# Performance work log

Hardware: AMD Instinct MI355X
Metric: run time of the kernel (lower is better)

Reference implementation:

```python
import jax, jax.numpy as jnp
import numpy as np

N = 50000
E = 800000
D = 128
NCLASS = 10


def setup_inputs() -> dict:
    key = jax.random.key(0)
    ks = jax.random.split(key, 12)
    stdv = 1.0 / np.sqrt(D)
    inp = {
        "x": jax.random.normal(ks[0], (N, D), dtype=jnp.float32),
        "edge_src": jax.random.randint(ks[1], (E,), 0, N, dtype=jnp.int32),
        "edge_dst": jax.random.randint(ks[2], (E,), 0, N, dtype=jnp.int32),
        "edge_weight": jax.random.uniform(ks[3], (E,), dtype=jnp.float32),
        "W1": jax.random.uniform(ks[4], (D, D), jnp.float32, -stdv, stdv),
        "b1": jax.random.uniform(ks[5], (D,), jnp.float32, -stdv, stdv),
        "W2": jax.random.uniform(ks[6], (D, D), jnp.float32, -stdv, stdv),
        "b2": jax.random.uniform(ks[7], (D,), jnp.float32, -stdv, stdv),
        "W3": jax.random.uniform(ks[8], (D, D), jnp.float32, -stdv, stdv),
        "b3": jax.random.uniform(ks[9], (D,), jnp.float32, -stdv, stdv),
        "lin_W": jax.random.normal(ks[10], (NCLASS, 3 * D), dtype=jnp.float32) * 0.05,
        "lin_b": jax.random.normal(ks[11], (NCLASS,), dtype=jnp.float32) * 0.05,
    }
    return inp


def _gcn_layer(h, W, b, edge_src, edge_dst, edge_weight):
    # support = h @ W  (dense GEMM), then spmm(adj, support) as gather-scale-scatter
    support = h @ W                                   # [N, out]
    msgs = support[edge_src] * edge_weight[:, None]   # [E, out]
    agg = jax.ops.segment_sum(msgs, edge_dst, num_segments=h.shape[0])
    return agg + b


def reference(x, edge_src, edge_dst, edge_weight, W1, b1, W2, b2, W3, b3, lin_W, lin_b):
    x1 = jax.nn.relu(_gcn_layer(x, W1, b1, edge_src, edge_dst, edge_weight))
    o1 = jnp.max(x1, axis=0)
    x2 = jax.nn.relu(_gcn_layer(x1, W2, b2, edge_src, edge_dst, edge_weight))
    o2 = jnp.max(x2, axis=0)
    x3 = _gcn_layer(x2, W3, b3, edge_src, edge_dst, edge_weight)
    o3 = jnp.max(x3, axis=0)
    lin_in = jnp.concatenate([o1, o2, o3], axis=0)    # [3*D]
    logits = lin_W @ lin_in + lin_b                   # [nclass]
    return jax.nn.log_softmax(logits, axis=0)
```

## Files before the change

### kernel.cpp

```cpp
#include <hip/hip_runtime.h>
#include <hip/hip_bf16.h>
#include <math.h>

#define NN 50000
#define NPAD 50048
#define NE 800000
#define DD 128
#define NCLS 10
#define SCAN_BLOCK 1024
#define NTILES ((NN + 1 + SCAN_BLOCK - 1) / SCAN_BLOCK)

typedef short s16x8 __attribute__((ext_vector_type(8)));
typedef float f32x4 __attribute__((ext_vector_type(4)));

__device__ __forceinline__ unsigned short f2bf(float x) {
  __hip_bfloat16 h = __float2bfloat16(x);
  return __builtin_bit_cast(unsigned short, h);
}

__device__ __forceinline__ unsigned int fkey(float f) {
  unsigned int u = __float_as_uint(f);
  return u ^ ((u & 0x80000000u) ? 0xFFFFFFFFu : 0x80000000u);
}
__device__ __forceinline__ float funkey(unsigned int k) {
  unsigned int u = (k & 0x80000000u) ? (k ^ 0x80000000u) : ~k;
  return __uint_as_float(u);
}

__global__ void k_init(int* __restrict__ offs, unsigned int* __restrict__ omax) {
  int i = blockIdx.x * blockDim.x + threadIdx.x;
  if (i < NN + 1) offs[i] = 0;
  if (i < 3 * DD) omax[i] = 0u;
}

__global__ void k_count(const int* __restrict__ edst, int* __restrict__ offs) {
  int e = blockIdx.x * blockDim.x + threadIdx.x;
  if (e < NE) atomicAdd(&offs[edst[e] + 1], 1);
}

__global__ void k_scan_partial(const int* __restrict__ offs, int* __restrict__ bsum) {
  __shared__ int red[SCAN_BLOCK];
  int i = blockIdx.x * SCAN_BLOCK + threadIdx.x;
  red[threadIdx.x] = (i < NN + 1) ? offs[i] : 0;
  __syncthreads();
  for (int off = SCAN_BLOCK / 2; off > 0; off >>= 1) {
    if ((int)threadIdx.x < off) red[threadIdx.x] += red[threadIdx.x + off];
    __syncthreads();
  }
  if (threadIdx.x == 0) bsum[blockIdx.x] = red[0];
}

__global__ void k_scan_bsum(int* __restrict__ bsum) {
  if (threadIdx.x == 0) {
    int run = 0;
    for (int i = 0; i < NTILES; ++i) { int v = bsum[i]; bsum[i] = run; run += v; }
  }
}

__global__ void k_scan_final(int* __restrict__ offs, const int* __restrict__ bsum,
                             int* __restrict__ cursor) {
  __shared__ int tmp[SCAN_BLOCK];
  int i = blockIdx.x * SCAN_BLOCK + threadIdx.x;
  int v = (i < NN + 1) ? offs[i] : 0;
  tmp[threadIdx.x] = v;
  __syncthreads();
  for (int off = 1; off < SCAN_BLOCK; off <<= 1) {
    int t = ((int)threadIdx.x >= off) ? tmp[threadIdx.x - off] : 0;
    __syncthreads();
    tmp[threadIdx.x] += t;
    __syncthreads();
  }
  int incl = tmp[threadIdx.x] + bsum[blockIdx.x];
  if (i < NN + 1) {
    offs[i] = incl;
    if (i < NN) cursor[i] = incl;
  }
}

__global__ void k_fill(const int* __restrict__ esrc, const int* __restrict__ edst,
                       const float* __restrict__ ew, int* __restrict__ cursor,
                       int2* __restrict__ csr) {
  int e = blockIdx.x * blockDim.x + threadIdx.x;
  if (e < NE) {
    int d = edst[e];
    int p = atomicAdd(&cursor[d], 1);
    csr[p] = make_int2(esrc[e], __float_as_int(ew[e]));
  }
}

__global__ __launch_bounds__(256) void k_cvt(const float* __restrict__ x,
                     const float* __restrict__ W1, const float* __restrict__ W2,
                     const float* __restrict__ W3,
                     unsigned short* __restrict__ HB,
                     unsigned short* __restrict__ WT1, unsigned short* __restrict__ WT2,
                     unsigned short* __restrict__ WT3) {
  const int stride = gridDim.x * 256;
  int i = blockIdx.x * 256 + threadIdx.x;
  const int n4 = NPAD * DD / 4;
  const int nx4 = NN * DD / 4;
  for (int idx = i; idx < n4; idx += stride) {
    float4 v = make_float4(0.f, 0.f, 0.f, 0.f);
    if (idx < nx4) v = ((const float4*)x)[idx];
    ushort2 lo = make_ushort2(f2bf(v.x), f2bf(v.y));
    ushort2 hi = make_ushort2(f2bf(v.z), f2bf(v.w));
    uint2 pv = make_uint2((uint)lo.x | ((uint)lo.y << 16), (uint)hi.x | ((uint)hi.y << 16));
    *(uint2*)&HB[idx * 4] = pv;
  }
  if (i < DD * DD) {
    int k = i >> 7, c = i & 127;
    WT1[c * DD + k] = f2bf(W1[i]);
    WT2[c * DD + k] = f2bf(W2[i]);
    WT3[c * DD + k] = f2bf(W3[i]);
  }
}

__global__ __launch_bounds__(256) void k_mm(const unsigned short* __restrict__ H,
                                            const unsigned short* __restrict__ Wt,
                                            unsigned short* __restrict__ S) {
  const int wave = threadIdx.x >> 6, lane = threadIdx.x & 63;
  const int gw = blockIdx.x * 4 + wave;
  const int r0 = (gw >> 1) * 64;
  const int cbase = (gw & 1) * 64;
  const int l15 = lane & 15, lk = (lane >> 4) * 8;

  s16x8 Af[4][4];
  s16x8 Bf[4][4];
#pragma unroll
  for (int m = 0; m < 4; ++m)
#pragma unroll
    for (int ks = 0; ks < 4; ++ks)
      Af[m][ks] = *(const s16x8*)&Wt[(cbase + m * 16 + l15) * DD + ks * 32 + lk];
#pragma unroll
  for (int n = 0; n < 4; ++n)
#pragma unroll
    for (int ks = 0; ks < 4; ++ks)
      Bf[n][ks] = *(const s16x8*)&H[(size_t)(r0 + n * 16 + l15) * DD + ks * 32 + lk];

  f32x4 acc[4][4];
#pragma unroll
  for (int m = 0; m < 4; ++m)
#pragma unroll
    for (int n = 0; n < 4; ++n) acc[m][n] = (f32x4){0.f, 0.f, 0.f, 0.f};

#pragma unroll
  for (int ks = 0; ks < 4; ++ks)
#pragma unroll
    for (int m = 0; m < 4; ++m)
#pragma unroll
      for (int n = 0; n < 4; ++n)
        acc[m][n] = __builtin_amdgcn_mfma_f32_16x16x32_bf16(Af[m][ks], Bf[n][ks],
                                                            acc[m][n], 0, 0, 0);

  const int csub = 4 * (lane >> 4);
#pragma unroll
  for (int m = 0; m < 4; ++m)
#pragma unroll
    for (int n = 0; n < 4; ++n) {
      uint2 pv;
      pv.x = (uint)f2bf(acc[m][n][0]) | ((uint)f2bf(acc[m][n][1]) << 16);
      pv.y = (uint)f2bf(acc[m][n][2]) | ((uint)f2bf(acc[m][n][3]) << 16);
      *(uint2*)&S[(size_t)(r0 + n * 16 + l15) * DD + cbase + m * 16 + csub] = pv;
    }
}

__global__ __launch_bounds__(256) void k_agg(const unsigned short* __restrict__ S,
                                             const int2* __restrict__ csr,
                                             const int* __restrict__ offs,
                                             const float* __restrict__ bias,
                                             unsigned short* __restrict__ Xout,
                                             unsigned int* __restrict__ omax,
                                             int do_relu) {
  __shared__ unsigned int cmax[DD];
  for (int i = threadIdx.x; i < DD; i += 256) cmax[i] = 0u;
  __syncthreads();
  const int lane = threadIdx.x & 63;
  const int wave = threadIdx.x >> 6;
  const int gwave = blockIdx.x * 4 + wave;
  const int nwaves = gridDim.x * 4;
  const int c0 = lane * 2;
  const float2 b2 = *(const float2*)&bias[c0];
  float2 mx = make_float2(-INFINITY, -INFINITY);
  for (int d = gwave; d < NN; d += nwaves) {
    const int e1 = offs[d + 1];
    int e = offs[d];
    float2 acc = b2;
    for (; e + 4 <= e1; e += 4) {
      int2 sw0 = csr[e + 0];
      int2 sw1 = csr[e + 1];
      int2 sw2 = csr[e + 2];
      int2 sw3 = csr[e + 3];
      unsigned int u0 = *(const unsigned int*)&S[(size_t)sw0.x * DD + c0];
      unsigned int u1 = *(const unsigned int*)&S[(size_t)sw1.x * DD + c0];
      unsigned int u2 = *(const unsigned int*)&S[(size_t)sw2.x * DD + c0];
      unsigned int u3 = *(const unsigned int*)&S[(size_t)sw3.x * DD + c0];
      float w0 = __int_as_float(sw0.y), w1 = __int_as_float(sw1.y);
      float w2 = __int_as_float(sw2.y), w3 = __int_as_float(sw3.y);
      acc.x = fmaf(w0, __uint_as_float(u0 << 16), acc.x);
      acc.y = fmaf(w0, __uint_as_float(u0 & 0xFFFF0000u), acc.y);
      acc.x = fmaf(w1, __uint_as_float(u1 << 16), acc.x);
      acc.y = fmaf(w1, __uint_as_float(u1 & 0xFFFF0000u), acc.y);
      acc.x = fmaf(w2, __uint_as_float(u2 << 16), acc.x);
      acc.y = fmaf(w2, __uint_as_float(u2 & 0xFFFF0000u), acc.y);
      acc.x = fmaf(w3, __uint_as_float(u3 << 16), acc.x);
      acc.y = fmaf(w3, __uint_as_float(u3 & 0xFFFF0000u), acc.y);
    }
    for (; e < e1; ++e) {
      int2 sw = csr[e];
      float w = __int_as_float(sw.y);
      unsigned int u = *(const unsigned int*)&S[(size_t)sw.x * DD + c0];
      acc.x = fmaf(w, __uint_as_float(u << 16), acc.x);
      acc.y = fmaf(w, __uint_as_float(u & 0xFFFF0000u), acc.y);
    }
    if (do_relu) { acc.x = fmaxf(acc.x, 0.f); acc.y = fmaxf(acc.y, 0.f); }
    if (Xout) {
      unsigned int xu = (unsigned int)f2bf(acc.x) | ((unsigned int)f2bf(acc.y) << 16);
      *(unsigned int*)&Xout[(size_t)d * DD + c0] = xu;
    }
    mx.x = fmaxf(mx.x, acc.x);
    mx.y = fmaxf(mx.y, acc.y);
  }
  atomicMax(&cmax[c0], fkey(mx.x));
  atomicMax(&cmax[c0 + 1], fkey(mx.y));
  __syncthreads();
  for (int i = threadIdx.x; i < DD; i += 256) atomicMax(&omax[i], cmax[i]);
}

__global__ void k_head(const unsigned int* __restrict__ omax,
                       const float* __restrict__ linW,
                       const float* __restrict__ linb,
                       float* __restrict__ out) {
  __shared__ float o[3 * DD];
  __shared__ float logits[NCLS];
  int t = threadIdx.x;
  if (t < 3 * DD) o[t] = funkey(omax[t]);
  __syncthreads();
  if (t < NCLS) {
    float acc = linb[t];
    for (int j = 0; j < 3 * DD; ++j) acc = fmaf(linW[t * 3 * DD + j], o[j], acc);
    logits[t] = acc;
  }
  __syncthreads();
  if (t == 0) {
    float m = -INFINITY;
    for (int c = 0; c < NCLS; ++c) m = fmaxf(m, logits[c]);
    float s = 0.f;
    for (int c = 0; c < NCLS; ++c) s += expf(logits[c] - m);
    float ls = logf(s);
    for (int c = 0; c < NCLS; ++c) out[c] = logits[c] - m - ls;
  }
}

extern "C" void kernel_launch(void* const* d_in, const int* in_sizes, int n_in,
                              void* d_out, int out_size, void* d_ws, size_t ws_size,
                              hipStream_t stream) {
  const float* x    = (const float*)d_in[0];
  const int*   esrc = (const int*)d_in[1];
  const int*   edst = (const int*)d_in[2];
  const float* ew   = (const float*)d_in[3];
  const float* W1   = (const float*)d_in[4];
  const float* b1   = (const float*)d_in[5];
  const float* W2   = (const float*)d_in[6];
  const float* b2   = (const float*)d_in[7];
  const float* W3   = (const float*)d_in[8];
  const float* b3   = (const float*)d_in[9];
  const float* linW = (const float*)d_in[10];
  const float* linb = (const float*)d_in[11];
  float* out = (float*)d_out;

  size_t off = 0;
  auto alloc = [&](size_t bytes) {
    void* p = (char*)d_ws + off;
    off += (bytes + 255) & ~(size_t)255;
    return p;
  };
  unsigned short* HB   = (unsigned short*)alloc((size_t)NPAD * DD * 2);
  unsigned short* XB   = (unsigned short*)alloc((size_t)NPAD * DD * 2);
  unsigned short* S    = (unsigned short*)alloc((size_t)NPAD * DD * 2);
  unsigned short* WT1  = (unsigned short*)alloc((size_t)DD * DD * 2);
  unsigned short* WT2  = (unsigned short*)alloc((size_t)DD * DD * 2);
  unsigned short* WT3  = (unsigned short*)alloc((size_t)DD * DD * 2);
  int*          offs   = (int*)alloc((NN + 1) * 4);
  int*          cursor = (int*)alloc(NN * 4);
  int2*         csr    = (int2*)alloc((size_t)NE * 8);
  unsigned int* omax   = (unsigned int*)alloc(3 * DD * 4);
  int*          bsum   = (int*)alloc(NTILES * 4);
  (void)ws_size; (void)n_in; (void)in_sizes; (void)out_size;

  k_init<<<(NN + 256) / 256, 256, 0, stream>>>(offs, omax);
  k_count<<<(NE + 255) / 256, 256, 0, stream>>>(edst, offs);
  k_scan_partial<<<NTILES, SCAN_BLOCK, 0, stream>>>(offs, bsum);
  k_scan_bsum<<<1, 64, 0, stream>>>(bsum);
  k_scan_final<<<NTILES, SCAN_BLOCK, 0, stream>>>(offs, bsum, cursor);
  k_fill<<<(NE + 255) / 256, 256, 0, stream>>>(esrc, edst, ew, cursor, csr);

  k_cvt<<<2048, 256, 0, stream>>>(x, W1, W2, W3, HB, WT1, WT2, WT3);

  const int mm_grid = (NPAD / 64) * 2 / 4;
  k_mm<<<mm_grid, 256, 0, stream>>>(HB, WT1, S);
  k_agg<<<2048, 256, 0, stream>>>(S, csr, offs, b1, XB, omax, 1);
  k_mm<<<mm_grid, 256, 0, stream>>>(XB, WT2, S);
  k_agg<<<2048, 256, 0, stream>>>(S, csr, offs, b2, HB, omax + DD, 1);
  k_mm<<<mm_grid, 256, 0, stream>>>(HB, WT3, S);
  k_agg<<<2048, 256, 0, stream>>>(S, csr, offs, b3, nullptr, omax + 2 * DD, 0);

  k_head<<<1, 384, 0, stream>>>(omax, linW, linb, out);
}
```

Baseline: 440.5 us.

## Fuse x bf16 conversion into GEMM, halve GEMM tile, widen aggregation gathers

Removes the separate pass that converts x to bf16 and folds that conversion into the first GEMM's operand load, which saves one full read and write of the node features. The GEMM tile per wave shrinks from 64 to 32 rows, doubling the grid and lowering register use. The aggregation kernel now gives each quarter-wave a different edge and has each lane gather 16 bytes, then combines the quarters with cross-lane shuffles. This trades a few shuffles per node and a ragged tail loop for fewer, wider gather transactions.

```diff
diff --git a/kernel.cpp b/kernel.cpp
--- a/kernel.cpp
+++ b/kernel.cpp
@@ -17,6 +17,8 @@
   __hip_bfloat16 h = __float2bfloat16(x);
   return __builtin_bit_cast(unsigned short, h);
 }
+__device__ __forceinline__ float bflo(unsigned int u) { return __uint_as_float(u << 16); }
+__device__ __forceinline__ float bfhi(unsigned int u) { return __uint_as_float(u & 0xFFFF0000u); }
 
 __device__ __forceinline__ unsigned int fkey(float f) {
   unsigned int u = __float_as_uint(f);
@@ -88,24 +90,11 @@
   }
 }
 
-__global__ __launch_bounds__(256) void k_cvt(const float* __restrict__ x,
-                     const float* __restrict__ W1, const float* __restrict__ W2,
-                     const float* __restrict__ W3,
-                     unsigned short* __restrict__ HB,
-                     unsigned short* __restrict__ WT1, unsigned short* __restrict__ WT2,
-                     unsigned short* __restrict__ WT3) {
-  const int stride = gridDim.x * 256;
+__global__ __launch_bounds__(256) void k_cvtW(const float* __restrict__ W1,
+    const float* __restrict__ W2, const float* __restrict__ W3,
+    unsigned short* __restrict__ WT1, unsigned short* __restrict__ WT2,
+    unsigned short* __restrict__ WT3) {
   int i = blockIdx.x * 256 + threadIdx.x;
-  const int n4 = NPAD * DD / 4;
-  const int nx4 = NN * DD / 4;
-  for (int idx = i; idx < n4; idx += stride) {
-    float4 v = make_float4(0.f, 0.f, 0.f, 0.f);
-    if (idx < nx4) v = ((const float4*)x)[idx];
-    ushort2 lo = make_ushort2(f2bf(v.x), f2bf(v.y));
-    ushort2 hi = make_ushort2(f2bf(v.z), f2bf(v.w));
-    uint2 pv = make_uint2((uint)lo.x | ((uint)lo.y << 16), (uint)hi.x | ((uint)hi.y << 16));
-    *(uint2*)&HB[idx * 4] = pv;
-  }
   if (i < DD * DD) {
     int k = i >> 7, c = i & 127;
     WT1[c * DD + k] = f2bf(W1[i]);
@@ -114,40 +103,63 @@
   }
 }
 
-__global__ __launch_bounds__(256) void k_mm(const unsigned short* __restrict__ H,
+template <int F32IN>
+__global__ __launch_bounds__(256) void k_mm(const void* __restrict__ Hv,
                                             const unsigned short* __restrict__ Wt,
                                             unsigned short* __restrict__ S) {
   const int wave = threadIdx.x >> 6, lane = threadIdx.x & 63;
   const int gw = blockIdx.x * 4 + wave;
-  const int r0 = (gw >> 1) * 64;
+  const int r0 = (gw >> 1) * 32;
   const int cbase = (gw & 1) * 64;
   const int l15 = lane & 15, lk = (lane >> 4) * 8;
 
   s16x8 Af[4][4];
-  s16x8 Bf[4][4];
 #pragma unroll
   for (int m = 0; m < 4; ++m)
 #pragma unroll
     for (int ks = 0; ks < 4; ++ks)
       Af[m][ks] = *(const s16x8*)&Wt[(cbase + m * 16 + l15) * DD + ks * 32 + lk];
-#pragma unroll
-  for (int n = 0; n < 4; ++n)
-#pragma unroll
-    for (int ks = 0; ks < 4; ++ks)
-      Bf[n][ks] = *(const s16x8*)&H[(size_t)(r0 + n * 16 + l15) * DD + ks * 32 + lk];
-
-  f32x4 acc[4][4];
+
+  s16x8 Bf[2][4];
+#pragma unroll
+  for (int n = 0; n < 2; ++n) {
+    const int r = r0 + n * 16 + l15;
+    if (F32IN) {
+      const float* H = (const float*)Hv;
+#pragma unroll
+      for (int ks = 0; ks < 4; ++ks) {
+        float4 a = make_float4(0.f, 0.f, 0.f, 0.f), b = a;
+        if (r < NN) {
+          a = *(const float4*)&H[(size_t)r * DD + ks * 32 + lk];
+          b = *(const float4*)&H[(size_t)r * DD + ks * 32 + lk + 4];
+        }
+        s16x8 f;
+        f[0] = (short)f2bf(a.x); f[1] = (short)f2bf(a.y);
+        f[2] = (short)f2bf(a.z); f[3] = (short)f2bf(a.w);
+        f[4] = (short)f2bf(b.x); f[5] = (short)f2bf(b.y);
+        f[6] = (short)f2bf(b.z); f[7] = (short)f2bf(b.w);
+        Bf[n][ks] = f;
+      }
+    } else {
+      const unsigned short* H = (const unsigned short*)Hv;
+#pragma unroll
+      for (int ks = 0; ks < 4; ++ks)
+        Bf[n][ks] = *(const s16x8*)&H[(size_t)r * DD + ks * 32 + lk];
+    }
+  }
+
+  f32x4 acc[4][2];
 #pragma unroll
   for (int m = 0; m < 4; ++m)
 #pragma unroll
-    for (int n = 0; n < 4; ++n) acc[m][n] = (f32x4){0.f, 0.f, 0.f, 0.f};
+    for (int n = 0; n < 2; ++n) acc[m][n] = (f32x4){0.f, 0.f, 0.f, 0.f};
 
 #pragma unroll
   for (int ks = 0; ks < 4; ++ks)
 #pragma unroll
     for (int m = 0; m < 4; ++m)
 #pragma unroll
-      for (int n = 0; n < 4; ++n)
+      for (int n = 0; n < 2; ++n)
         acc[m][n] = __builtin_amdgcn_mfma_f32_16x16x32_bf16(Af[m][ks], Bf[n][ks],
                                                             acc[m][n], 0, 0, 0);
 
@@ -155,12 +167,23 @@
 #pragma unroll
   for (int m = 0; m < 4; ++m)
 #pragma unroll
-    for (int n = 0; n < 4; ++n) {
+    for (int n = 0; n < 2; ++n) {
       uint2 pv;
       pv.x = (uint)f2bf(acc[m][n][0]) | ((uint)f2bf(acc[m][n][1]) << 16);
       pv.y = (uint)f2bf(acc[m][n][2]) | ((uint)f2bf(acc[m][n][3]) << 16);
       *(uint2*)&S[(size_t)(r0 + n * 16 + l15) * DD + cbase + m * 16 + csub] = pv;
     }
+}
+
+__device__ __forceinline__ void fma8(float* acc, float w, uint4 u) {
+  acc[0] = fmaf(w, bflo(u.x), acc[0]);
+  acc[1] = fmaf(w, bfhi(u.x), acc[1]);
+  acc[2] = fmaf(w, bflo(u.y), acc[2]);
+  acc[3] = fmaf(w, bfhi(u.y), acc[3]);
+  acc[4] = fmaf(w, bflo(u.z), acc[4]);
+  acc[5] = fmaf(w, bfhi(u.z), acc[5]);
+  acc[6] = fmaf(w, bflo(u.w), acc[6]);
+  acc[7] = fmaf(w, bfhi(u.w), acc[7]);
 }
 
 __global__ __launch_bounds__(256) void k_agg(const unsigned short* __restrict__ S,
@@ -175,52 +198,70 @@
   __syncthreads();
   const int lane = threadIdx.x & 63;
   const int wave = threadIdx.x >> 6;
+  const int q = lane >> 4;
+  const int t = lane & 15;
   const int gwave = blockIdx.x * 4 + wave;
   const int nwaves = gridDim.x * 4;
-  const int c0 = lane * 2;
-  const float2 b2 = *(const float2*)&bias[c0];
-  float2 mx = make_float2(-INFINITY, -INFINITY);
+
+  float bcol[8];
+  {
+    float4 b0 = *(const float4*)&bias[t * 8];
+    float4 b1 = *(const float4*)&bias[t * 8 + 4];
+    bcol[0] = b0.x; bcol[1] = b0.y; bcol[2] = b0.z; bcol[3] = b0.w;
+    bcol[4] = b1.x; bcol[5] = b1.y; bcol[6] = b1.z; bcol[7] = b1.w;
+  }
+  float mx[8];
+#pragma unroll
+  for (int j = 0; j < 8; ++j) mx[j] = -INFINITY;
+
   for (int d = gwave; d < NN; d += nwaves) {
-    const int e1 = offs[d + 1];
-    int e = offs[d];
-    float2 acc = b2;
-    for (; e + 4 <= e1; e += 4) {
-      int2 sw0 = csr[e + 0];
-      int2 sw1 = csr[e + 1];
-      int2 sw2 = csr[e + 2];
-      int2 sw3 = csr[e + 3];
-      unsigned int u0 = *(const unsigned int*)&S[(size_t)sw0.x * DD + c0];
-      unsigned int u1 = *(const unsigned int*)&S[(size_t)sw1.x * DD + c0];
-      unsigned int u2 = *(const unsigned int*)&S[(size_t)sw2.x * DD + c0];
-      unsigned int u3 = *(const unsigned int*)&S[(size_t)sw3.x * DD + c0];
-      float w0 = __int_as_float(sw0.y), w1 = __int_as_float(sw1.y);
-      float w2 = __int_as_float(sw2.y), w3 = __int_as_float(sw3.y);
-      acc.x = fmaf(w0, __uint_as_float(u0 << 16), acc.x);
-      acc.y = fmaf(w0, __uint_as_float(u0 & 0xFFFF0000u), acc.y);
-      acc.x = fmaf(w1, __uint_as_float(u1 << 16), acc.x);
-      acc.y = fmaf(w1, __uint_as_float(u1 & 0xFFFF0000u), acc.y);
-      acc.x = fmaf(w2, __uint_as_float(u2 << 16), acc.x);
-      acc.y = fmaf(w2, __uint_as_float(u2 & 0xFFFF0000u), acc.y);
-      acc.x = fmaf(w3, __uint_as_float(u3 << 16), acc.x);
-      acc.y = fmaf(w3, __uint_as_float(u3 & 0xFFFF0000u), acc.y);
-    }
-    for (; e < e1; ++e) {
-      int2 sw = csr[e];
-      float w = __int_as_float(sw.y);
-      unsigned int u = *(const unsigned int*)&S[(size_t)sw.x * DD + c0];
-      acc.x = fmaf(w, __uint_as_float(u << 16), acc.x);
-      acc.y = fmaf(w, __uint_as_float(u & 0xFFFF0000u), acc.y);
-    }
-    if (do_relu) { acc.x = fmaxf(acc.x, 0.f); acc.y = fmaxf(acc.y, 0.f); }
-    if (Xout) {
-      unsigned int xu = (unsigned int)f2bf(acc.x) | ((unsigned int)f2bf(acc.y) << 16);
-      *(unsigned int*)&Xout[(size_t)d * DD + c0] = xu;
-    }
-    mx.x = fmaxf(mx.x, acc.x);
-    mx.y = fmaxf(mx.y, acc.y);
-  }
-  atomicMax(&cmax[c0], fkey(mx.x));
-  atomicMax(&cmax[c0 + 1], fkey(mx.y));
+    const int e0 = offs[d], e1 = offs[d + 1];
+    float acc[8] = {0.f, 0.f, 0.f, 0.f, 0.f, 0.f, 0.f, 0.f};
+    int e = e0 + q;
+    const int nfull = (e1 - e0) >> 4;
+    for (int s = 0; s < nfull; ++s, e += 16) {
+      int2 c0 = csr[e];
+      int2 c1 = csr[e + 4];
+      int2 c2 = csr[e + 8];
+      int2 c3 = csr[e + 12];
+      uint4 u0 = *(const uint4*)&S[(size_t)c0.x * DD + t * 8];
+      uint4 u1 = *(const uint4*)&S[(size_t)c1.x * DD + t * 8];
+      uint4 u2 = *(const uint4*)&S[(size_t)c2.x * DD + t * 8];
+      uint4 u3 = *(const uint4*)&S[(size_t)c3.x * DD + t * 8];
+      fma8(acc, __int_as_float(c0.y), u0);
+      fma8(acc, __int_as_float(c1.y), u1);
+      fma8(acc, __int_as_float(c2.y), u2);
+      fma8(acc, __int_as_float(c3.y), u3);
+    }
+    while (__any(e < e1)) {
+      if (e < e1) {
+        int2 c = csr[e];
+        uint4 u = *(const uint4*)&S[(size_t)c.x * DD + t * 8];
+        fma8(acc, __int_as_float(c.y), u);
+      }
+      e += 4;
+    }
+#pragma unroll
+    for (int j = 0; j < 8; ++j) {
+      acc[j] += __shfl_xor(acc[j], 16, 64);
+      acc[j] += __shfl_xor(acc[j], 32, 64);
+      acc[j] += bcol[j];
+      if (do_relu) acc[j] = fmaxf(acc[j], 0.f);
+      mx[j] = fmaxf(mx[j], acc[j]);
+    }
+    if (Xout && q == 0) {
+      uint4 xv;
+      xv.x = (uint)f2bf(acc[0]) | ((uint)f2bf(acc[1]) << 16);
+      xv.y = (uint)f2bf(acc[2]) | ((uint)f2bf(acc[3]) << 16);
+      xv.z = (uint)f2bf(acc[4]) | ((uint)f2bf(acc[5]) << 16);
+      xv.w = (uint)f2bf(acc[6]) | ((uint)f2bf(acc[7]) << 16);
+      *(uint4*)&Xout[(size_t)d * DD + t * 8] = xv;
+    }
+  }
+  if (q == 0) {
+#pragma unroll
+    for (int j = 0; j < 8; ++j) atomicMax(&cmax[t * 8 + j], fkey(mx[j]));
+  }
   __syncthreads();
   for (int i = threadIdx.x; i < DD; i += 256) atomicMax(&omax[i], cmax[i]);
 }
@@ -273,8 +314,8 @@
     off += (bytes + 255) & ~(size_t)255;
     return p;
   };
-  unsigned short* HB   = (unsigned short*)alloc((size_t)NPAD * DD * 2);
-  unsigned short* XB   = (unsigned short*)alloc((size_t)NPAD * DD * 2);
+  unsigned short* X1   = (unsigned short*)alloc((size_t)NPAD * DD * 2);
+  unsigned short* X2   = (unsigned short*)alloc((size_t)NPAD * DD * 2);
   unsigned short* S    = (unsigned short*)alloc((size_t)NPAD * DD * 2);
   unsigned short* WT1  = (unsigned short*)alloc((size_t)DD * DD * 2);
   unsigned short* WT2  = (unsigned short*)alloc((size_t)DD * DD * 2);
@@ -293,14 +334,14 @@
   k_scan_final<<<NTILES, SCAN_BLOCK, 0, stream>>>(offs, bsum, cursor);
   k_fill<<<(NE + 255) / 256, 256, 0, stream>>>(esrc, edst, ew, cursor, csr);
 
-  k_cvt<<<2048, 256, 0, stream>>>(x, W1, W2, W3, HB, WT1, WT2, WT3);
-
-  const int mm_grid = (NPAD / 64) * 2 / 4;
-  k_mm<<<mm_grid, 256, 0, stream>>>(HB, WT1, S);
-  k_agg<<<2048, 256, 0, stream>>>(S, csr, offs, b1, XB, omax, 1);
-  k_mm<<<mm_grid, 256, 0, stream>>>(XB, WT2, S);
-  k_agg<<<2048, 256, 0, stream>>>(S, csr, offs, b2, HB, omax + DD, 1);
-  k_mm<<<mm_grid, 256, 0, stream>>>(HB, WT3, S);
+  k_cvtW<<<(DD * DD + 255) / 256, 256, 0, stream>>>(W1, W2, W3, WT1, WT2, WT3);
+
+  const int mm_grid = (NPAD / 32) * 2 / 4;
+  k_mm<1><<<mm_grid, 256, 0, stream>>>(x, WT1, S);
+  k_agg<<<2048, 256, 0, stream>>>(S, csr, offs, b1, X1, omax, 1);
+  k_mm<0><<<mm_grid, 256, 0, stream>>>(X1, WT2, S);
+  k_agg<<<2048, 256, 0, stream>>>(S, csr, offs, b2, X2, omax + DD, 1);
+  k_mm<0><<<mm_grid, 256, 0, stream>>>(X2, WT3, S);
   k_agg<<<2048, 256, 0, stream>>>(S, csr, offs, b3, nullptr, omax + 2 * DD, 0);
 
   k_head<<<1, 384, 0, stream>>>(omax, linW, linb, out);
```

Measured after the change: 438.6 us. Within noise of the previous version (-0.4%).
